# Kernel tuning notes

Measured on AMD Instinct MI355X. Metric: run time of the kernel, lower is better.

The kernel has to match this reference:

```python
import jax, jax.numpy as jnp
import numpy as np

B, S, H, NH = 4, 2048, 2048, 16
HD = H // NH
EPS = 1e-5


def setup_inputs() -> dict:
    key = jax.random.key(0)
    ks = jax.random.split(key, 5)
    return {
        "x": jax.random.normal(ks[0], (B, S, H), dtype=jnp.float32),
        "ln_w": jnp.ones((H,), dtype=jnp.float32),
        "ln_b": jnp.zeros((H,), dtype=jnp.float32),
        "c_attn_w": jax.random.normal(ks[1], (H, 3 * H), dtype=jnp.float32) * 0.02,
        "c_attn_b": jax.random.normal(ks[2], (3 * H,), dtype=jnp.float32) * 0.02,
        "c_proj_w": jax.random.normal(ks[3], (H, H), dtype=jnp.float32) * 0.02,
        "c_proj_b": jax.random.normal(ks[4], (H,), dtype=jnp.float32) * 0.02,
    }


def reference(x, ln_w, ln_b, c_attn_w, c_attn_b, c_proj_w, c_proj_b):
    residual = x
    # fused layer norm
    mu = jnp.mean(x, axis=-1, keepdims=True)
    var = jnp.mean(jnp.square(x - mu), axis=-1, keepdims=True)
    xn = (x - mu) * jax.lax.rsqrt(var + EPS) * ln_w + ln_b
    qkv = jnp.einsum("bsh,hk->bsk", xn, c_attn_w) + c_attn_b
    q, k, v = jnp.split(qkv, 3, axis=-1)
    def heads(t):
        return t.reshape(B, S, NH, HD).transpose(0, 2, 1, 3)
    q, k, v = heads(q), heads(k), heads(v)
    # causal flash attention (reference math)
    scale = 1.0 / np.sqrt(HD)
    scores = jnp.einsum("bnqd,bnkd->bnqk", q, k) * scale
    causal = jnp.tril(jnp.ones((S, S), dtype=bool))
    scores = jnp.where(causal, scores, jnp.finfo(scores.dtype).min)
    attn = jax.nn.softmax(scores, axis=-1)
    o = jnp.einsum("bnqk,bnkd->bnqd", attn, v)
    # merge heads: [B,NH,S,HD] -> [B,S,H]
    o = o.transpose(0, 2, 1, 3).reshape(B, S, H)
    # output projection + residual (fused_ffn, add_gelu=False, dropout=0)
    return jnp.einsum("bsh,hk->bsk", o, c_proj_w) + c_proj_b + residual
```

## Files before the change

### kernel.cpp

```cpp
#include <hip/hip_runtime.h>
#include <stdint.h>
#include <math.h>

#define B_  4
#define S_  2048
#define H_  2048
#define NH_ 16
#define HD_ 128
#define M_  (B_*S_)
#define N3_ (3*H_)
#define NQT_ (S_/64)

typedef __attribute__((ext_vector_type(8))) short short8;
typedef __attribute__((ext_vector_type(4))) float floatx4;

__device__ __forceinline__ unsigned short f2bf(float f) {
  unsigned u = __float_as_uint(f);
  u += 0x7FFF + ((u >> 16) & 1);
  return (unsigned short)(u >> 16);
}

__global__ __launch_bounds__(256) void ln_kernel(
    const float* __restrict__ x, const float* __restrict__ w,
    const float* __restrict__ b, unsigned short* __restrict__ xn) {
  int row = blockIdx.x;
  int t = threadIdx.x;
  const float* xr = x + (size_t)row * H_;
  float4 v0 = *(const float4*)(xr + t * 4);
  float4 v1 = *(const float4*)(xr + 1024 + t * 4);
  float s  = v0.x + v0.y + v0.z + v0.w + v1.x + v1.y + v1.z + v1.w;
  float sq = v0.x*v0.x + v0.y*v0.y + v0.z*v0.z + v0.w*v0.w
           + v1.x*v1.x + v1.y*v1.y + v1.z*v1.z + v1.w*v1.w;
  #pragma unroll
  for (int m = 32; m; m >>= 1) { s += __shfl_xor(s, m); sq += __shfl_xor(sq, m); }
  __shared__ float red[8];
  int wv = t >> 6;
  if ((t & 63) == 0) { red[wv * 2] = s; red[wv * 2 + 1] = sq; }
  __syncthreads();
  s  = red[0] + red[2] + red[4] + red[6];
  sq = red[1] + red[3] + red[5] + red[7];
  float mu  = s * (1.0f / H_);
  float var = sq * (1.0f / H_) - mu * mu;
  float rs  = rsqrtf(var + 1e-5f);

  float4 w0 = *(const float4*)(w + t * 4);
  float4 b0 = *(const float4*)(b + t * 4);
  float4 w1 = *(const float4*)(w + 1024 + t * 4);
  float4 b1 = *(const float4*)(b + 1024 + t * 4);
  ushort4 o0, o1;
  o0.x = f2bf((v0.x - mu) * rs * w0.x + b0.x);
  o0.y = f2bf((v0.y - mu) * rs * w0.y + b0.y);
  o0.z = f2bf((v0.z - mu) * rs * w0.z + b0.z);
  o0.w = f2bf((v0.w - mu) * rs * w0.w + b0.w);
  o1.x = f2bf((v1.x - mu) * rs * w1.x + b1.x);
  o1.y = f2bf((v1.y - mu) * rs * w1.y + b1.y);
  o1.z = f2bf((v1.z - mu) * rs * w1.z + b1.z);
  o1.w = f2bf((v1.w - mu) * rs * w1.w + b1.w);
  unsigned short* orow = xn + (size_t)row * H_;
  *(ushort4*)(orow + t * 4) = o0;
  *(ushort4*)(orow + 1024 + t * 4) = o1;
}

__global__ __launch_bounds__(256) void transpose_f2b(
    const float* __restrict__ in, unsigned short* __restrict__ out,
    int R, int C) {
  __shared__ float tile[32][33];
  int tx = threadIdx.x & 31, ty = threadIdx.x >> 5;
  int c0 = blockIdx.x * 32, r0 = blockIdx.y * 32;
  #pragma unroll
  for (int i = 0; i < 32; i += 8)
    tile[ty + i][tx] = in[(size_t)(r0 + ty + i) * C + c0 + tx];
  __syncthreads();
  #pragma unroll
  for (int i = 0; i < 32; i += 8)
    out[(size_t)(c0 + ty + i) * R + r0 + tx] = f2bf(tile[tx][ty + i]);
}

__global__ __launch_bounds__(256) void qkv_gemm(
    const unsigned short* __restrict__ A, const unsigned short* __restrict__ Bt,
    const float* __restrict__ bias,
    unsigned short* __restrict__ qw, unsigned short* __restrict__ kw,
    unsigned short* __restrict__ vtw) {
  __shared__ unsigned short As[128 * 72];
  __shared__ unsigned short Bs[128 * 72];
  int n0 = blockIdx.x * 128, m0 = blockIdx.y * 128;
  int t = threadIdx.x, lane = t & 63, wv = t >> 6;
  int l15 = lane & 15, quad = lane >> 4;
  int wm = wv >> 1, wn = wv & 1;
  floatx4 acc[4][4];
  #pragma unroll
  for (int i = 0; i < 4; i++)
    #pragma unroll
    for (int j = 0; j < 4; j++) acc[i][j] = (floatx4){0.f, 0.f, 0.f, 0.f};

  int sr = t >> 3, sc = (t & 7) * 8;
  for (int k0 = 0; k0 < H_; k0 += 64) {
    __syncthreads();
    #pragma unroll
    for (int c = 0; c < 4; c++) {
      int row = c * 32 + sr;
      *(short8*)(As + row * 72 + sc) =
          *(const short8*)(A + (size_t)(m0 + row) * H_ + k0 + sc);
      *(short8*)(Bs + row * 72 + sc) =
          *(const short8*)(Bt + (size_t)(n0 + row) * H_ + k0 + sc);
    }
    __syncthreads();
    #pragma unroll
    for (int ks = 0; ks < 2; ks++) {
      short8 af[4], bf[4];
      #pragma unroll
      for (int i = 0; i < 4; i++)
        af[i] = *(const short8*)(As + (wm * 64 + i * 16 + l15) * 72 + ks * 32 + quad * 8);
      #pragma unroll
      for (int j = 0; j < 4; j++)
        bf[j] = *(const short8*)(Bs + (wn * 64 + j * 16 + l15) * 72 + ks * 32 + quad * 8);
      #pragma unroll
      for (int i = 0; i < 4; i++)
        #pragma unroll
        for (int j = 0; j < 4; j++)
          acc[i][j] = __builtin_amdgcn_mfma_f32_16x16x32_bf16(af[i], bf[j], acc[i][j], 0, 0, 0);
    }
  }
  int sec = n0 >> 11;
  int h = (n0 >> 7) & 15;
  #pragma unroll
  for (int j = 0; j < 4; j++) {
    int d = wn * 64 + j * 16 + l15;
    float bval = bias[n0 + d];
    #pragma unroll
    for (int i = 0; i < 4; i++) {
      #pragma unroll
      for (int reg = 0; reg < 4; reg++) {
        int m = m0 + wm * 64 + i * 16 + quad * 4 + reg;
        unsigned short bv = f2bf(acc[i][j][reg] + bval);
        int bb = m >> 11, s = m & 2047;
        int bh = bb * NH_ + h;
        if (sec == 0)      qw[((size_t)bh * S_ + s) * HD_ + d] = bv;
        else if (sec == 1) kw[((size_t)bh * S_ + s) * HD_ + d] = bv;
        else               vtw[((size_t)bh * HD_ + d) * S_ + s] = bv;
      }
    }
  }
}

__global__ __launch_bounds__(256) void proj_gemm(
    const unsigned short* __restrict__ A, const unsigned short* __restrict__ Bt,
    const float* __restrict__ bias, const float* __restrict__ resid,
    float* __restrict__ out) {
  __shared__ unsigned short As[128 * 72];
  __shared__ unsigned short Bs[128 * 72];
  int n0 = blockIdx.x * 128, m0 = blockIdx.y * 128;
  int t = threadIdx.x, lane = t & 63, wv = t >> 6;
  int l15 = lane & 15, quad = lane >> 4;
  int wm = wv >> 1, wn = wv & 1;
  floatx4 acc[4][4];
  #pragma unroll
  for (int i = 0; i < 4; i++)
    #pragma unroll
    for (int j = 0; j < 4; j++) acc[i][j] = (floatx4){0.f, 0.f, 0.f, 0.f};

  int sr = t >> 3, sc = (t & 7) * 8;
  for (int k0 = 0; k0 < H_; k0 += 64) {
    __syncthreads();
    #pragma unroll
    for (int c = 0; c < 4; c++) {
      int row = c * 32 + sr;
      *(short8*)(As + row * 72 + sc) =
          *(const short8*)(A + (size_t)(m0 + row) * H_ + k0 + sc);
      *(short8*)(Bs + row * 72 + sc) =
          *(const short8*)(Bt + (size_t)(n0 + row) * H_ + k0 + sc);
    }
    __syncthreads();
    #pragma unroll
    for (int ks = 0; ks < 2; ks++) {
      short8 af[4], bf[4];
      #pragma unroll
      for (int i = 0; i < 4; i++)
        af[i] = *(const short8*)(As + (wm * 64 + i * 16 + l15) * 72 + ks * 32 + quad * 8);
      #pragma unroll
      for (int j = 0; j < 4; j++)
        bf[j] = *(const short8*)(Bs + (wn * 64 + j * 16 + l15) * 72 + ks * 32 + quad * 8);
      #pragma unroll
      for (int i = 0; i < 4; i++)
        #pragma unroll
        for (int j = 0; j < 4; j++)
          acc[i][j] = __builtin_amdgcn_mfma_f32_16x16x32_bf16(af[i], bf[j], acc[i][j], 0, 0, 0);
    }
  }
  #pragma unroll
  for (int j = 0; j < 4; j++) {
    int n = n0 + wn * 64 + j * 16 + l15;
    float bval = bias[n];
    #pragma unroll
    for (int i = 0; i < 4; i++) {
      #pragma unroll
      for (int reg = 0; reg < 4; reg++) {
        int m = m0 + wm * 64 + i * 16 + quad * 4 + reg;
        out[(size_t)m * H_ + n] = acc[i][j][reg] + bval + resid[(size_t)m * H_ + n];
      }
    }
  }
}

__global__ __launch_bounds__(256) void attn_kernel(
    const unsigned short* __restrict__ qw, const unsigned short* __restrict__ kw,
    const unsigned short* __restrict__ vtw, unsigned short* __restrict__ ow) {
  __shared__ unsigned short Klds[64 * 136];
  __shared__ unsigned short Vtl[128 * 72];
  __shared__ unsigned short Pl[4][16 * 72];
  int pr = blockIdx.x, bh = blockIdx.y;
  int t = threadIdx.x, lane = t & 63, wv = t >> 6;
  int l15 = lane & 15, quad = lane >> 4;
  int h = bh & 15, bb = bh >> 4;

  const float scale = 0.08838834764831845f;
  int krr = t >> 4, kcc = (t & 15) * 8;
  int vdd = t >> 3, vss = (t & 7) * 8;
  unsigned short* plw = &Pl[wv][0];
  const unsigned short* kgb = kw + ((size_t)bh * S_ + krr) * HD_ + kcc;
  const unsigned short* vgb = vtw + ((size_t)bh * HD_ + vdd) * S_ + vss;

  short8 kreg[4], vreg[4];
  auto load_stage = [&](int kb) {
    #pragma unroll
    for (int c = 0; c < 4; c++) {
      kreg[c] = *(const short8*)(kgb + (size_t)(kb + c * 16) * HD_);
      vreg[c] = *(const short8*)(vgb + (size_t)(c * 32) * S_ + kb);
    }
  };

  #pragma unroll 1
  for (int half = 0; half < 2; half++) {
    int qt = half ? (NQT_ - 1 - pr) : pr;
    int qr = qt * 64 + wv * 16;
    int q = qr + l15;

    short8 qf[4];
    {
      const unsigned short* qbase = qw + ((size_t)bh * S_ + q) * HD_ + quad * 8;
      #pragma unroll
      for (int ks = 0; ks < 4; ks++)
        qf[ks] = *(const short8*)(qbase + ks * 32);
    }

    float m_i = -INFINITY, l_i = 0.f;
    floatx4 o[8];
    #pragma unroll
    for (int ht = 0; ht < 8; ht++) o[ht] = (floatx4){0.f, 0.f, 0.f, 0.f};

    load_stage(0);
    #pragma unroll 1
    for (int kt = 0; kt <= qt; kt++) {
      int kb = kt * 64;
      __syncthreads();
      #pragma unroll
      for (int c = 0; c < 4; c++) {
        *(short8*)(Klds + (c * 16 + krr) * 136 + kcc) = kreg[c];
        *(short8*)(Vtl + (c * 32 + vdd) * 72 + vss) = vreg[c];
      }
      __syncthreads();
      if (kt < qt) load_stage(kb + 64);

      floatx4 sv[4];
      #pragma unroll
      for (int jm = 0; jm < 4; jm++) {
        sv[jm] = (floatx4){0.f, 0.f, 0.f, 0.f};
        #pragma unroll
        for (int ks = 0; ks < 4; ks++) {
          short8 kf = *(const short8*)(Klds + (jm * 16 + l15) * 136 + ks * 32 + quad * 8);
          sv[jm] = __builtin_amdgcn_mfma_f32_16x16x32_bf16(kf, qf[ks], sv[jm], 0, 0, 0);
        }
      }

      float p[4][4];
      float mx = m_i;
      #pragma unroll
      for (int jm = 0; jm < 4; jm++)
        #pragma unroll
        for (int reg = 0; reg < 4; reg++) {
          float v = sv[jm][reg] * scale;
          int key = kb + jm * 16 + quad * 4 + reg;
          if (key > q) v = -1e30f;
          p[jm][reg] = v;
          mx = fmaxf(mx, v);
        }
      mx = fmaxf(mx, __shfl_xor(mx, 16));
      mx = fmaxf(mx, __shfl_xor(mx, 32));
      float sum = 0.f;
      #pragma unroll
      for (int jm = 0; jm < 4; jm++)
        #pragma unroll
        for (int reg = 0; reg < 4; reg++) { p[jm][reg] = __expf(p[jm][reg] - mx); sum += p[jm][reg]; }
      sum += __shfl_xor(sum, 16);
      sum += __shfl_xor(sum, 32);
      float alpha = __expf(m_i - mx);
      l_i = l_i * alpha + sum;
      m_i = mx;
      #pragma unroll
      for (int ht = 0; ht < 8; ht++) o[ht] *= alpha;

      #pragma unroll
      for (int jm = 0; jm < 4; jm++) {
        ushort4 pk;
        pk.x = f2bf(p[jm][0]); pk.y = f2bf(p[jm][1]);
        pk.z = f2bf(p[jm][2]); pk.w = f2bf(p[jm][3]);
        *(ushort4*)(plw + l15 * 72 + jm * 16 + quad * 4) = pk;
      }

      #pragma unroll
      for (int ks2 = 0; ks2 < 2; ks2++) {
        short8 pf = *(const short8*)(plw + l15 * 72 + ks2 * 32 + quad * 8);
        #pragma unroll
        for (int ht = 0; ht < 8; ht++) {
          short8 vf = *(const short8*)(Vtl + (ht * 16 + l15) * 72 + ks2 * 32 + quad * 8);
          o[ht] = __builtin_amdgcn_mfma_f32_16x16x32_bf16(vf, pf, o[ht], 0, 0, 0);
        }
      }
    }

    float inv = 1.0f / l_i;
    size_t base = ((size_t)(bb * S_ + q)) * H_ + h * HD_ + quad * 4;
    #pragma unroll
    for (int ht = 0; ht < 8; ht++) {
      ushort4 ov;
      ov.x = f2bf(o[ht][0] * inv); ov.y = f2bf(o[ht][1] * inv);
      ov.z = f2bf(o[ht][2] * inv); ov.w = f2bf(o[ht][3] * inv);
      *(ushort4*)(ow + base + ht * 16) = ov;
    }
  }
}

extern "C" void kernel_launch(void* const* d_in, const int* in_sizes, int n_in,
                              void* d_out, int out_size, void* d_ws, size_t ws_size,
                              hipStream_t stream) {
  (void)in_sizes; (void)n_in; (void)out_size; (void)ws_size;
  const float* x      = (const float*)d_in[0];
  const float* ln_w   = (const float*)d_in[1];
  const float* ln_b   = (const float*)d_in[2];
  const float* attn_w = (const float*)d_in[3];
  const float* attn_b = (const float*)d_in[4];
  const float* proj_w = (const float*)d_in[5];
  const float* proj_b = (const float*)d_in[6];
  float* out = (float*)d_out;

  char* ws = (char*)d_ws;
  size_t off = 0;
  auto alloc = [&](size_t bytes) {
    char* p = ws + off;
    off += (bytes + 255) & ~(size_t)255;
    return p;
  };
  unsigned short* xn     = (unsigned short*)alloc((size_t)M_ * H_ * 2);
  unsigned short* wqkvt  = (unsigned short*)alloc((size_t)N3_ * H_ * 2);
  unsigned short* wprojt = (unsigned short*)alloc((size_t)H_ * H_ * 2);
  unsigned short* qws    = (unsigned short*)alloc((size_t)M_ * H_ * 2);
  unsigned short* kws    = (unsigned short*)alloc((size_t)M_ * H_ * 2);
  unsigned short* vtws   = (unsigned short*)alloc((size_t)M_ * H_ * 2);
  unsigned short* attn_out = xn;

  ln_kernel<<<M_, 256, 0, stream>>>(x, ln_w, ln_b, xn);
  transpose_f2b<<<dim3(N3_ / 32, H_ / 32), 256, 0, stream>>>(attn_w, wqkvt, H_, N3_);
  transpose_f2b<<<dim3(H_ / 32, H_ / 32), 256, 0, stream>>>(proj_w, wprojt, H_, H_);
  qkv_gemm<<<dim3(N3_ / 128, M_ / 128), 256, 0, stream>>>(xn, wqkvt, attn_b, qws, kws, vtws);
  attn_kernel<<<dim3(NQT_ / 2, B_ * NH_), 256, 0, stream>>>(qws, kws, vtws, attn_out);
  proj_gemm<<<dim3(H_ / 128, M_ / 128), 256, 0, stream>>>(attn_out, wprojt, proj_b, x, out);
}
```

Baseline: 736.8 us.

## Use direct global-to-LDS loads in GEMMs and vectorize V-transpose stores

Result: no change. 727.0 us (-1.3%).

```diff
diff --git a/kernel.cpp b/kernel.cpp
--- a/kernel.cpp
+++ b/kernel.cpp
@@ -13,11 +13,18 @@
 
 typedef __attribute__((ext_vector_type(8))) short short8;
 typedef __attribute__((ext_vector_type(4))) float floatx4;
+typedef unsigned int u32;
 
 __device__ __forceinline__ unsigned short f2bf(float f) {
   unsigned u = __float_as_uint(f);
   u += 0x7FFF + ((u >> 16) & 1);
   return (unsigned short)(u >> 16);
+}
+
+__device__ __forceinline__ void gl2lds16(const void* g, void* l) {
+  __builtin_amdgcn_global_load_lds(
+      (const __attribute__((address_space(1))) u32*)g,
+      (__attribute__((address_space(3))) u32*)l, 16, 0, 0);
 }
 
 __global__ __launch_bounds__(256) void ln_kernel(
@@ -81,8 +88,8 @@
     const float* __restrict__ bias,
     unsigned short* __restrict__ qw, unsigned short* __restrict__ kw,
     unsigned short* __restrict__ vtw) {
-  __shared__ unsigned short As[128 * 72];
-  __shared__ unsigned short Bs[128 * 72];
+  __shared__ unsigned short As[128 * 64];
+  __shared__ unsigned short Bs[128 * 64];
   int n0 = blockIdx.x * 128, m0 = blockIdx.y * 128;
   int t = threadIdx.x, lane = t & 63, wv = t >> 6;
   int l15 = lane & 15, quad = lane >> 4;
@@ -93,16 +100,17 @@
     #pragma unroll
     for (int j = 0; j < 4; j++) acc[i][j] = (floatx4){0.f, 0.f, 0.f, 0.f};
 
-  int sr = t >> 3, sc = (t & 7) * 8;
+  const unsigned short* ag = A + (size_t)(m0 + (t >> 3)) * H_ + (t & 7) * 8;
+  const unsigned short* bg = Bt + (size_t)(n0 + (t >> 3)) * H_ + (t & 7) * 8;
+  unsigned short* asl = As + t * 8;
+  unsigned short* bsl = Bs + t * 8;
+
   for (int k0 = 0; k0 < H_; k0 += 64) {
     __syncthreads();
     #pragma unroll
     for (int c = 0; c < 4; c++) {
-      int row = c * 32 + sr;
-      *(short8*)(As + row * 72 + sc) =
-          *(const short8*)(A + (size_t)(m0 + row) * H_ + k0 + sc);
-      *(short8*)(Bs + row * 72 + sc) =
-          *(const short8*)(Bt + (size_t)(n0 + row) * H_ + k0 + sc);
+      gl2lds16(ag + (size_t)(c * 32) * H_ + k0, asl + c * 2048);
+      gl2lds16(bg + (size_t)(c * 32) * H_ + k0, bsl + c * 2048);
     }
     __syncthreads();
     #pragma unroll
@@ -110,10 +118,10 @@
       short8 af[4], bf[4];
       #pragma unroll
       for (int i = 0; i < 4; i++)
-        af[i] = *(const short8*)(As + (wm * 64 + i * 16 + l15) * 72 + ks * 32 + quad * 8);
+        af[i] = *(const short8*)(As + (wm * 64 + i * 16 + l15) * 64 + ks * 32 + quad * 8);
       #pragma unroll
       for (int j = 0; j < 4; j++)
-        bf[j] = *(const short8*)(Bs + (wn * 64 + j * 16 + l15) * 72 + ks * 32 + quad * 8);
+        bf[j] = *(const short8*)(Bs + (wn * 64 + j * 16 + l15) * 64 + ks * 32 + quad * 8);
       #pragma unroll
       for (int i = 0; i < 4; i++)
         #pragma unroll
@@ -129,15 +137,19 @@
     float bval = bias[n0 + d];
     #pragma unroll
     for (int i = 0; i < 4; i++) {
-      #pragma unroll
-      for (int reg = 0; reg < 4; reg++) {
-        int m = m0 + wm * 64 + i * 16 + quad * 4 + reg;
-        unsigned short bv = f2bf(acc[i][j][reg] + bval);
-        int bb = m >> 11, s = m & 2047;
-        int bh = bb * NH_ + h;
-        if (sec == 0)      qw[((size_t)bh * S_ + s) * HD_ + d] = bv;
-        else if (sec == 1) kw[((size_t)bh * S_ + s) * HD_ + d] = bv;
-        else               vtw[((size_t)bh * HD_ + d) * S_ + s] = bv;
+      int m = m0 + wm * 64 + i * 16 + quad * 4;
+      int bb = m >> 11, s = m & 2047;
+      int bh = bb * NH_ + h;
+      if (sec == 2) {
+        ushort4 pv;
+        pv.x = f2bf(acc[i][j][0] + bval); pv.y = f2bf(acc[i][j][1] + bval);
+        pv.z = f2bf(acc[i][j][2] + bval); pv.w = f2bf(acc[i][j][3] + bval);
+        *(ushort4*)(vtw + ((size_t)bh * HD_ + d) * S_ + s) = pv;
+      } else {
+        unsigned short* dst = (sec == 0 ? qw : kw) + ((size_t)bh * S_ + s) * HD_ + d;
+        #pragma unroll
+        for (int reg = 0; reg < 4; reg++)
+          dst[(size_t)reg * HD_] = f2bf(acc[i][j][reg] + bval);
       }
     }
   }
@@ -147,8 +159,8 @@
     const unsigned short* __restrict__ A, const unsigned short* __restrict__ Bt,
     const float* __restrict__ bias, const float* __restrict__ resid,
     float* __restrict__ out) {
-  __shared__ unsigned short As[128 * 72];
-  __shared__ unsigned short Bs[128 * 72];
+  __shared__ unsigned short As[128 * 64];
+  __shared__ unsigned short Bs[128 * 64];
   int n0 = blockIdx.x * 128, m0 = blockIdx.y * 128;
   int t = threadIdx.x, lane = t & 63, wv = t >> 6;
   int l15 = lane & 15, quad = lane >> 4;
@@ -159,16 +171,17 @@
     #pragma unroll
     for (int j = 0; j < 4; j++) acc[i][j] = (floatx4){0.f, 0.f, 0.f, 0.f};
 
-  int sr = t >> 3, sc = (t & 7) * 8;
+  const unsigned short* ag = A + (size_t)(m0 + (t >> 3)) * H_ + (t & 7) * 8;
+  const unsigned short* bg = Bt + (size_t)(n0 + (t >> 3)) * H_ + (t & 7) * 8;
+  unsigned short* asl = As + t * 8;
+  unsigned short* bsl = Bs + t * 8;
+
   for (int k0 = 0; k0 < H_; k0 += 64) {
     __syncthreads();
     #pragma unroll
     for (int c = 0; c < 4; c++) {
-      int row = c * 32 + sr;
-      *(short8*)(As + row * 72 + sc) =
-          *(const short8*)(A + (size_t)(m0 + row) * H_ + k0 + sc);
-      *(short8*)(Bs + row * 72 + sc) =
-          *(const short8*)(Bt + (size_t)(n0 + row) * H_ + k0 + sc);
+      gl2lds16(ag + (size_t)(c * 32) * H_ + k0, asl + c * 2048);
+      gl2lds16(bg + (size_t)(c * 32) * H_ + k0, bsl + c * 2048);
     }
     __syncthreads();
     #pragma unroll
@@ -176,10 +189,10 @@
       short8 af[4], bf[4];
       #pragma unroll
       for (int i = 0; i < 4; i++)
-        af[i] = *(const short8*)(As + (wm * 64 + i * 16 + l15) * 72 + ks * 32 + quad * 8);
+        af[i] = *(const short8*)(As + (wm * 64 + i * 16 + l15) * 64 + ks * 32 + quad * 8);
       #pragma unroll
       for (int j = 0; j < 4; j++)
-        bf[j] = *(const short8*)(Bs + (wn * 64 + j * 16 + l15) * 72 + ks * 32 + quad * 8);
+        bf[j] = *(const short8*)(Bs + (wn * 64 + j * 16 + l15) * 64 + ks * 32 + quad * 8);
       #pragma unroll
       for (int i = 0; i < 4; i++)
         #pragma unroll
```
